# Kernel tuning notes

Hardware: AMD Instinct MI355X
Metric: run time of the kernel (lower is better)

Reference implementation:

```python
import jax, jax.numpy as jnp
import numpy as np

EPS = 1e-5


def _conv1x1_3d(x, w, b):
    # x: [B,C,T,H,W], w: [O,C], b: [O]  (Conv3d with kernel 1)
    return jnp.einsum('bcthw,oc->bothw', x, w) + b[None, :, None, None, None]


def _nonlocal_layer(x, Kw, Kb, Qw, Qb, Vw, Vb, Ow, Ob, gamma, beta, in_dim):
    K = _conv1x1_3d(x, Kw, Kb)
    Q = _conv1x1_3d(x, Qw, Qb)
    V = _conv1x1_3d(x, Vw, Vb)
    B, C, T, H, W = K.shape
    S = T * H * W
    Kf = K.reshape(B, C, S)
    Qf = Q.reshape(B, C, S)
    Vf = V.reshape(B, C, S)
    # KQ[b,s,t] = sum_c K[b,c,s] Q[b,c,t];  attn = softmax over t
    attn = jax.nn.softmax(jnp.einsum('bcs,bct->bst', Kf, Qf) / np.sqrt(in_dim).astype(np.float32), axis=2)
    # original broadcast pattern: (V.view(B,C,S,1) * attn[:,None]).sum(3)
    #   == V[b,c,s] * sum_t attn[b,s,t]  (rows of softmax sum to ~1)
    Vn = Vf * attn.sum(axis=2)[:, None, :]
    Vn = jax.nn.relu(Vn).reshape(B, C, T, H, W)
    O = jax.nn.relu(_conv1x1_3d(Vn, Ow, Ob))
    y = x + O
    # BatchNorm3d in training mode: per-channel batch statistics
    mu = y.mean(axis=(0, 2, 3, 4), keepdims=True)
    var = y.var(axis=(0, 2, 3, 4), keepdims=True)
    return gamma[None, :, None, None, None] * (y - mu) / jnp.sqrt(var + EPS) + beta[None, :, None, None, None]


def _conv_transpose_2x2_s2(x, w, b):
    # torch ConvTranspose2d(k=2, stride=2): weight [Cin, Cout, 2, 2]; output pixels don't overlap
    N, C, H, W = x.shape
    O = w.shape[1]
    y = jnp.einsum('nchw,codk->nohdwk', x, w).reshape(N, O, 2 * H, 2 * W)
    return y + b[None, :, None, None]


def _positional_encoding(S, D):
    position = jnp.arange(S, dtype=jnp.float32)[:, None]
    div_term = jnp.exp(jnp.arange(0, D, 2, dtype=jnp.float32) * (-np.log(10000.0) / D))
    pe = jnp.zeros((S, D), dtype=jnp.float32)
    pe = pe.at[:, 0::2].set(jnp.sin(position * div_term))
    pe = pe.at[:, 1::2].set(jnp.cos(position * div_term))
    return pe  # [S, D]


def setup_inputs() -> dict:
    key = jax.random.key(0)
    ks = jax.random.split(key, 24)
    B, Tc, Hc, Wc = 8, 6, 12, 12
    Tf, Hf, Wf = 4, 12, 12
    Din, Dff, Dout, L = 1024, 512, 128, 2
    s = 0.02
    inp = {
        'context': jax.random.normal(ks[0], (B, Tc, Din, Hc, Wc), jnp.float32),
        'frame': jax.random.normal(ks[1], (B, Tf, Din, Hf, Wf), jnp.float32),
        'nl_Kw': jax.random.normal(ks[2], (L, Dff, Din), jnp.float32) * s,
        'nl_Kb': jnp.zeros((L, Dff), jnp.float32),
        'nl_Qw': jax.random.normal(ks[3], (L, Dff, Din), jnp.float32) * s,
        'nl_Qb': jnp.zeros((L, Dff), jnp.float32),
        'nl_Vw': jax.random.normal(ks[4], (L, Dff, Din), jnp.float32) * s,
        'nl_Vb': jnp.zeros((L, Dff), jnp.float32),
        'nl_Ow': jax.random.normal(ks[5], (L, Din, Dff), jnp.float32) * s,
        'nl_Ob': jnp.zeros((L, Din), jnp.float32),
        'nl_gamma': jnp.ones((L, Din), jnp.float32),
        'nl_beta': jnp.zeros((L, Din), jnp.float32),
        'tp_w': jax.random.normal(ks[6], (Dout, Din, 3, 3, 3), jnp.float32) * s,
        'tp_b': jnp.zeros((Dout,), jnp.float32),
        'up1_w': jax.random.normal(ks[7], (Din, Dff, 2, 2), jnp.float32) * s,
        'up1_b': jnp.zeros((Dff,), jnp.float32),
        'up2_w': jax.random.normal(ks[8], (Dff, Dout, 2, 2), jnp.float32) * s,
        'up2_b': jnp.zeros((Dout,), jnp.float32),
    }
    return inp


def reference(context, frame, nl_Kw, nl_Kb, nl_Qw, nl_Qb, nl_Vw, nl_Vb, nl_Ow, nl_Ob,
              nl_gamma, nl_beta, tp_w, tp_b, up1_w, up1_b, up2_w, up2_b):
    in_dim = context.shape[2]
    out_dim = up2_w.shape[1]
    # ---- non-local layers over context ----
    x = jnp.swapaxes(context, 1, 2)  # [B, C, T, H, W]
    n_layers = nl_Kw.shape[0]
    for l in range(n_layers):
        x = _nonlocal_layer(x, nl_Kw[l], nl_Kb[l], nl_Qw[l], nl_Qb[l], nl_Vw[l], nl_Vb[l],
                            nl_Ow[l], nl_Ob[l], nl_gamma[l], nl_beta[l], in_dim)
    # ---- temporal pool (Conv3d k=3, VALID) + ReLU + global avg pool ----
    g = jax.lax.conv_general_dilated(x, tp_w, (1, 1, 1), 'VALID',
                                     dimension_numbers=('NCDHW', 'OIDHW', 'NCDHW'))
    g = jax.nn.relu(g + tp_b[None, :, None, None, None])
    goal_embed = g.mean(axis=(2, 3, 4))  # [B, out_dim]
    # ---- upsample frame ----
    B, Tf, C, H, W = frame.shape
    fr = frame.reshape(B * Tf, C, H, W)
    h = jax.nn.relu(_conv_transpose_2x2_s2(fr, up1_w, up1_b))
    h = _conv_transpose_2x2_s2(h, up2_w, up2_b)  # [B*Tf, out_dim, 4H, 4W]
    N = B * Tf
    S = H * W * 16
    state_embed = h.reshape(N, out_dim, S)
    # ---- positional encoding on V ----
    pe = _positional_encoding(S, out_dim)  # [S, D]
    V = jnp.transpose(state_embed, (0, 2, 1)) + pe[None, :, :]  # [N, S, D]
    # ---- goal/state attention (note: torch .repeat tiles t-major, kept faithful) ----
    goal_rep = jnp.tile(goal_embed, (Tf, 1))  # [Tf*B, D], index t*B+b
    SG = jnp.einsum('nds,nd->ns', state_embed, goal_rep) / np.sqrt(out_dim).astype(np.float32)
    attn = jax.nn.softmax(SG, axis=1)  # [N, S]
    state_goal_attn = jnp.einsum('ns,nsd->nd', attn, V).reshape(B, Tf, out_dim)
    return (goal_embed, state_goal_attn)
```

## Files before the change

### kernel.cpp

```cpp
#include <hip/hip_runtime.h>
#include <cstddef>
#include <cstdint>


static constexpr int B_ = 8, TC = 6, TF = 4, DIN = 1024, DFF = 512, DOUT = 128;
static constexpr int HWP = 144;
static constexpr int P_CTX = B_ * TC * HWP;
static constexpr int NF = B_ * TF;
static constexpr int P_FRM = NF * HWP;
static constexpr int P_H1 = NF * 24 * 24;
static constexpr int P_H2 = NF * 48 * 48;
static constexpr int S2 = 48 * 48;
static constexpr int NPOS = 3200;

static constexpr size_t OFF_XB   = 0;
static constexpr size_t OFF_YB   = 3538944;
static constexpr size_t OFF_VNB  = 7077888;
static constexpr size_t OFF_WB1  = 8847360;
static constexpr size_t OFF_WB2  = 9371648;
static constexpr size_t OFF_ST   = 9895936;
static constexpr size_t OFF_TWB  = 9900032;
static constexpr size_t OFF_W1B  = 11669504;
static constexpr size_t OFF_W2B  = 12718080;
static constexpr size_t OFF_GP   = 12849152;
static constexpr size_t OFF_R    = 18378752;
static constexpr size_t OFF_HP1B = 18788352;
static constexpr size_t OFF_F0B  = 23506944;
static constexpr size_t OFF_HP2B = 0;
static constexpr size_t OFF_SG   = 12849152;
static constexpr size_t OFF_PE   = 7077888;

typedef __attribute__((ext_vector_type(8))) short bf16x8;
typedef __attribute__((ext_vector_type(4))) float f32x4;
typedef __attribute__((ext_vector_type(4))) unsigned short us4;
typedef __attribute__((ext_vector_type(8))) unsigned short us8;

__device__ __forceinline__ unsigned short f2b(float f) {
    union { float f; uint32_t u; } x{f};
    uint32_t r = x.u + 0x7FFFu + ((x.u >> 16) & 1u);
    return (unsigned short)(r >> 16);
}
__device__ __forceinline__ float b2f(unsigned short u) {
    union { uint32_t u; float f; } x;
    x.u = (uint32_t)u << 16;
    return x.f;
}

#define GL16(g, s)                                                        \
    __builtin_amdgcn_global_load_lds(                                     \
        (const __attribute__((address_space(1))) void*)(g),               \
        (__attribute__((address_space(3))) void*)(s), 16, 0, 0)

static constexpr int PW0 = 4 * 524288;
static constexpr int PW1 = PW0 + 27 * 1024 * 128;
static constexpr int PW2 = PW1 + 4 * 512 * 1024;
static constexpr int PW3 = PW2 + 4 * 128 * 512;
static constexpr int NB_PREP = PW3 / 256;
static constexpr int NB_CTXT = 9 * 16 * (B_ * TC);
static constexpr int NB_FRMT = 9 * 16 * NF;

__device__ __forceinline__ void transpose_body(const float* __restrict__ in,
                                               unsigned short* __restrict__ outB,
                                               int C, int HW, int bx, int by, int bz,
                                               float (*T)[17]) {
    int tid = threadIdx.x;
    int tx = tid & 15, ty = tid >> 4;
    int f = bz, hw0 = bx * 16, c0 = by * 64;
#pragma unroll
    for (int i = 0; i < 4; ++i)
        T[ty + 16 * i][tx] = in[((size_t)f * C + c0 + ty + 16 * i) * HW + hw0 + tx];
    __syncthreads();
#pragma unroll
    for (int i = 0; i < 4; ++i)
        outB[((size_t)f * HW + hw0 + ty) * C + c0 + tx + 16 * i] = f2b(T[tx + 16 * i][ty]);
}

__global__ __launch_bounds__(256) void prep_all(
    const float* __restrict__ Vw, const float* __restrict__ Ow,
    const float* __restrict__ tp, const float* __restrict__ u1w,
    const float* __restrict__ u2w,
    const float* __restrict__ context, const float* __restrict__ frame,
    unsigned short* __restrict__ WB1, unsigned short* __restrict__ WB2,
    unsigned short* __restrict__ TWB, unsigned short* __restrict__ W1B,
    unsigned short* __restrict__ W2B,
    unsigned short* __restrict__ XB, unsigned short* __restrict__ F0B) {
    __shared__ float T[64][17];
    int b = blockIdx.x;
    if (b < NB_PREP) {
        int t = b * 256 + threadIdx.x;
        if (t < PW0) {
            int which = t >> 19;
            int r = t & 524287;
            int kr = r & 7;
            int layer = which >> 1;
            if ((which & 1) == 0) {
                int o = (r >> 3) & 511, kg = (r >> 3) >> 9;
                WB1[(size_t)layer * 524288 + r] =
                    f2b(Vw[(size_t)layer * 524288 + (size_t)o * 1024 + kg * 8 + kr]);
            } else {
                int o = (r >> 3) & 1023, kg = (r >> 3) >> 10;
                WB2[(size_t)layer * 524288 + r] =
                    f2b(Ow[(size_t)layer * 524288 + (size_t)o * 512 + kg * 8 + kr]);
            }
        } else if (t < PW1) {
            int r = t - PW0;
            int kr = r & 7, o = (r >> 3) & 127, kg = (r >> 10) & 127, tap = r >> 17;
            int c = kg * 8 + kr;
            TWB[r] = f2b(tp[((size_t)o * 1024 + c) * 27 + tap]);
        } else if (t < PW2) {
            int r = t - PW1;
            int kr = r & 7, o = (r >> 3) % 512;
            int rest = (r >> 3) / 512;
            int kg = rest & 127, d = rest >> 7;
            W1B[r] = f2b(u1w[((size_t)(kg * 8 + kr) * 512 + o) * 4 + d]);
        } else if (t < PW3) {
            int r = t - PW2;
            int kr = r & 7, o = (r >> 3) & 127;
            int rest = (r >> 3) >> 7;
            int kg = rest & 63, d = rest >> 6;
            W2B[r] = f2b(u2w[((size_t)(kg * 8 + kr) * 128 + o) * 4 + d]);
        }
    } else if (b < NB_PREP + NB_CTXT) {
        int bb = b - NB_PREP;
        transpose_body(context, XB, DIN, HWP, bb % 9, (bb / 9) % 16, bb / 144, T);
    } else {
        int bb = b - NB_PREP - NB_CTXT;
        transpose_body(frame, F0B, DIN, HWP, bb % 9, (bb / 9) % 16, bb / 144, T);
    }
}

template <int EPI, int REMAP, int GATHER, int MT>
__device__ __forceinline__ void gemm_body(
    const unsigned short* __restrict__ A, const unsigned short* __restrict__ Bp,
    const float* __restrict__ bias, const unsigned short* __restrict__ resid,
    void* __restrict__ Cv, int M, int N, int K,
    size_t bStrideZ, size_t cStrideZ,
    int inW, int inHW, int outW, int outSPP,
    int bx, int by, int bz,
    unsigned short* AlP, unsigned short* BlP, int* sPix) {
    constexpr int MI = MT / 32;
    constexpr int AL = MT / 64;
    constexpr int ASZ = MT * 32;
    int tid = threadIdx.x;
    int w = tid >> 6, l = tid & 63;
    int m0 = by * MT, n0 = bx * 128;
    int z = bz;
    const unsigned short* Bpz = Bp + (size_t)z * bStrideZ;

    if (GATHER) {
        if (tid < MT) {
            int pos = m0 + tid;
            int ww = pos % 10;
            int r = pos / 10;
            int h = r % 10;
            r /= 10;
            int t = r & 3, b = r >> 2;
            int dt = z / 9, rr = z - dt * 9;
            int doff = dt * 144 + (rr / 3) * 12 + (rr % 3);
            sPix[tid] = ((b * 6 + t) * 12 + h) * 12 + ww + doff;
        }
        __syncthreads();
    }

    int wr = w >> 1, wc = w & 1;
    int l15 = l & 15, lg = l >> 4;

    float bv[4];
#pragma unroll
    for (int ni = 0; ni < 4; ++ni)
        bv[ni] = (EPI & 1) ? bias[n0 + wc * 64 + ni * 16 + l15] : 0.f;
    asm volatile("s_waitcnt vmcnt(0)" ::: "memory");

    const unsigned short* ag[AL];
    int aoff[AL];
#pragma unroll
    for (int a = 0; a < AL; ++a) {
        int row = l + a * 64;
        int grow = GATHER ? sPix[row] : (m0 + row);
        ag[a] = A + (size_t)grow * K + w * 8;
        aoff[a] = (w * MT + row) * 8;
    }
    int bkg = tid >> 7, bn = tid & 127;
    const unsigned short* bg0 = Bpz + ((size_t)bkg * N + n0 + bn) * 8;
    const unsigned short* bg1 = Bpz + ((size_t)(bkg + 2) * N + n0 + bn) * 8;
    const int boff0 = tid * 8, boff1 = (tid + 256) * 8;
    size_t bstep = (size_t)32 * N;

    f32x4 acc[MI][4];
#pragma unroll
    for (int mi = 0; mi < MI; ++mi)
#pragma unroll
        for (int ni = 0; ni < 4; ++ni) acc[mi][ni] = (f32x4){0.f, 0.f, 0.f, 0.f};

    int nt = K >> 5;
#pragma unroll
    for (int a = 0; a < AL; ++a) { GL16(ag[a], &AlP[aoff[a]]); ag[a] += 32; }
    GL16(bg0, &BlP[boff0]);
    GL16(bg1, &BlP[boff1]);
    bg0 += bstep; bg1 += bstep;
#pragma unroll
    for (int a = 0; a < AL; ++a) { GL16(ag[a], &AlP[ASZ + aoff[a]]); ag[a] += 32; }
    GL16(bg0, &BlP[4096 + boff0]);
    GL16(bg1, &BlP[4096 + boff1]);
    bg0 += bstep; bg1 += bstep;

    int bc = 0, sb = 2;
    for (int t = 0; t < nt; ++t) {
        __builtin_amdgcn_s_barrier();
        if (t + 2 < nt) {
#pragma unroll
            for (int a = 0; a < AL; ++a) { GL16(ag[a], &AlP[sb * ASZ + aoff[a]]); ag[a] += 32; }
            GL16(bg0, &BlP[sb * 4096 + boff0]);
            GL16(bg1, &BlP[sb * 4096 + boff1]);
            bg0 += bstep; bg1 += bstep;
            if (MT == 128)
                asm volatile("s_waitcnt vmcnt(8)" ::: "memory");
            else
                asm volatile("s_waitcnt vmcnt(6)" ::: "memory");
        } else if (t + 2 == nt) {
            if (MT == 128)
                asm volatile("s_waitcnt vmcnt(4)" ::: "memory");
            else
                asm volatile("s_waitcnt vmcnt(3)" ::: "memory");
        } else {
            asm volatile("s_waitcnt vmcnt(0)" ::: "memory");
        }
        __builtin_amdgcn_sched_barrier(0);
        bf16x8 af[MI], bf[4];
#pragma unroll
        for (int mi = 0; mi < MI; ++mi)
            af[mi] = *(const bf16x8*)&AlP[bc * ASZ + (lg * MT + wr * (MT / 2) + mi * 16 + l15) * 8];
#pragma unroll
        for (int ni = 0; ni < 4; ++ni)
            bf[ni] = *(const bf16x8*)&BlP[bc * 4096 + (lg * 128 + wc * 64 + ni * 16 + l15) * 8];
        __builtin_amdgcn_s_setprio(1);
#pragma unroll
        for (int mi = 0; mi < MI; ++mi)
#pragma unroll
            for (int ni = 0; ni < 4; ++ni)
                acc[mi][ni] = __builtin_amdgcn_mfma_f32_16x16x32_bf16(
                    af[mi], bf[ni], acc[mi][ni], 0, 0, 0);
        __builtin_amdgcn_s_setprio(0);
        __builtin_amdgcn_sched_barrier(0);
        bc = (bc == 2) ? 0 : bc + 1;
        sb = (sb == 2) ? 0 : sb + 1;
    }

    float* Cf = (float*)Cv + (size_t)z * cStrideZ;
    unsigned short* Cb = (unsigned short*)Cv + (size_t)z * cStrideZ;
#pragma unroll
    for (int mi = 0; mi < MI; ++mi) {
#pragma unroll
        for (int r = 0; r < 4; ++r) {
            int m = m0 + wr * (MT / 2) + mi * 16 + lg * 4 + r;
            int orow = m;
            if (REMAP) {
                int ni_ = m / inHW;
                int rem = m - ni_ * inHW;
                int h = rem / inW, ww = rem - h * inW;
                orow = ni_ * outSPP + (2 * h + (z >> 1)) * outW + (2 * ww + (z & 1));
            }
#pragma unroll
            for (int ni = 0; ni < 4; ++ni) {
                int n = n0 + wc * 64 + ni * 16 + l15;
                float v = acc[mi][ni][r] + bv[ni];
                if (EPI & 2) v = fmaxf(v, 0.f);
                if (EPI & 4) v += b2f(resid[(size_t)m * N + n]);
                if (EPI & 8)
                    Cb[(size_t)orow * N + n] = f2b(v);
                else
                    Cf[(size_t)orow * N + n] = v;
            }
        }
    }
}

template <int EPI, int REMAP, int GATHER, int MT>
__global__ __launch_bounds__(256) void gemm_mfma(
    const unsigned short* __restrict__ A, const unsigned short* __restrict__ Bp,
    const float* __restrict__ bias, const unsigned short* __restrict__ resid,
    void* __restrict__ Cv, int M, int N, int K,
    size_t bStrideZ, size_t cStrideZ,
    int inW, int inHW, int outW, int outSPP) {
    __shared__ unsigned short Al[3 * MT * 32];
    __shared__ unsigned short Bl[3 * 128 * 32];
    __shared__ int sPix[MT];
    gemm_body<EPI, REMAP, GATHER, MT>(A, Bp, bias, resid, Cv, M, N, K,
                                      bStrideZ, cStrideZ, inW, inHW, outW, outSPP,
                                      blockIdx.x, blockIdx.y, blockIdx.z,
                                      Al, Bl, sPix);
}

__global__ __launch_bounds__(256) void conv3_up1(
    const unsigned short* __restrict__ XB, const unsigned short* __restrict__ TWB,
    unsigned short* __restrict__ GP,
    const unsigned short* __restrict__ F0B, const unsigned short* __restrict__ W1B,
    const float* __restrict__ u1b, unsigned short* __restrict__ HP1B) {
    __shared__ unsigned short Al[3 * 128 * 32];
    __shared__ unsigned short Bl[3 * 128 * 32];
    __shared__ int sPix[128];
    if (blockIdx.x < 680) {
        int xcd = blockIdx.x & 7, k = blockIdx.x >> 3;
        int wcnt = (xcd < 3) ? 85 : 84;
        if (k >= wcnt) return;
        int wk = (xcd < 3) ? xcd * 85 + k : 255 + (xcd - 3) * 84 + k;
        gemm_body<8, 0, 1, 128>(XB, TWB, nullptr, nullptr, GP, NPOS, DOUT, DIN,
                                (size_t)DIN / 8 * DOUT * 8, (size_t)NPOS * DOUT,
                                0, 0, 0, 0, 0, wk / 27, wk % 27, Al, Bl, sPix);
    } else {
        int b = blockIdx.x - 680;
        gemm_body<11, 1, 0, 128>(F0B, W1B, u1b, nullptr, HP1B, P_FRM, DFF, DIN,
                                 (size_t)DIN / 8 * DFF * 8, 0, 12, 144, 24, 576,
                                 b & 3, (b >> 2) % 36, b / 144, Al, Bl, sPix);
    }
}

__global__ __launch_bounds__(256) void up2_tail(
    const unsigned short* __restrict__ HP1B, const unsigned short* __restrict__ W2B,
    const float* __restrict__ u2b, unsigned short* __restrict__ HP2B,
    const unsigned short* __restrict__ Gp, const float* __restrict__ tpb,
    float* __restrict__ R, float* __restrict__ PE) {
    __shared__ unsigned short Al[3 * 128 * 32];
    __shared__ unsigned short Bl[3 * 128 * 32];
    __shared__ int sPix[128];
    int b = blockIdx.x;
    if (b < 576) {
        gemm_body<9, 1, 0, 128>(HP1B, W2B, u2b, nullptr, HP2B, P_H1, DOUT, DFF,
                                (size_t)DFF / 8 * DOUT * 8, 0, 24, 576, 48, 2304,
                                0, b % 144, b / 144, Al, Bl, sPix);
    } else if (b < 2176) {
        int idx = (b - 576) * 256 + threadIdx.x;
        float s = 0.f;
        for (int tap = 0; tap < 27; ++tap) s += b2f(Gp[(size_t)tap * (NPOS * 128) + idx]);
        R[idx] = fmaxf(s + tpb[idx & 127], 0.f);
    } else {
        int idx = (b - 2176) * 256 + threadIdx.x;
        int s = idx >> 7, d = idx & 127;
        float freq = expf(-(float)(d & ~1) * (9.210340371976184f / 128.f));
        float ang = (float)s * freq;
        PE[idx] = (d & 1) ? cosf(ang) : sinf(ang);
    }
}

__global__ __launch_bounds__(128) void goal_reduce(const float* __restrict__ R,
                                                   float* __restrict__ out) {
    int b = blockIdx.x, o = threadIdx.x;
    float s = 0.f;
    for (int i = 0; i < 400; ++i) s += R[(size_t)(b * 400 + i) * 128 + o];
    out[b * 128 + o] = s * (1.f / 400.f);
}


__global__ __launch_bounds__(256) void bn_stats_b(const unsigned short* __restrict__ YB,
                                                  float* __restrict__ st) {
    int tid = threadIdx.x;
    int p0 = blockIdx.x * 64;
    int c0 = tid * 4;
    float s[4] = {0, 0, 0, 0}, q[4] = {0, 0, 0, 0};
    for (int pp = 0; pp < 64; ++pp) {
        us4 y = *(const us4*)(YB + (size_t)(p0 + pp) * 1024 + c0);
#pragma unroll
        for (int j = 0; j < 4; ++j) {
            float v = b2f(y[j]);
            s[j] += v;
            q[j] += v * v;
        }
    }
#pragma unroll
    for (int j = 0; j < 4; ++j) {
        atomicAdd(&st[c0 + j], s[j]);
        atomicAdd(&st[1024 + c0 + j], q[j]);
    }
}

__global__ __launch_bounds__(256) void bn_final(float* __restrict__ st,
                                                const float* __restrict__ gamma,
                                                const float* __restrict__ beta) {
    int c = blockIdx.x * 256 + threadIdx.x;
    if (c >= 1024) return;
    const float invn = 1.f / 6912.f;
    float mean = st[c] * invn;
    float var = st[1024 + c] * invn - mean * mean;
    float sc = gamma[c] * rsqrtf(var + 1e-5f);
    st[2048 + c] = sc;
    st[3072 + c] = beta[c] - mean * sc;
}

__global__ __launch_bounds__(256) void bn_apply_b(const unsigned short* __restrict__ YB,
                                                  unsigned short* __restrict__ XB,
                                                  const float* __restrict__ st) {
    const float* scale = st + 2048;
    const float* shift = st + 3072;
    int idx = blockIdx.x * 256 + threadIdx.x;
    int c0 = (idx & 255) << 2;
    us4 y = ((const us4*)YB)[idx];
    us4 o;
#pragma unroll
    for (int j = 0; j < 4; ++j) o[j] = f2b(b2f(y[j]) * scale[c0 + j] + shift[c0 + j]);
    ((us4*)XB)[idx] = o;
}


__global__ __launch_bounds__(256) void attn_logits(const unsigned short* __restrict__ Hp2,
                                                   const float* __restrict__ out,
                                                   float* __restrict__ SG) {
    int n = blockIdx.y;
    int tid = threadIdx.x;
    int s = blockIdx.x * 16 + (tid >> 4);
    int l16 = tid & 15;
    us8 row = *((const us8*)(Hp2 + ((size_t)n * S2 + s) * 128) + l16);
    const float* g = out + (n & 7) * 128 + l16 * 8;
    float dot = 0.f;
#pragma unroll
    for (int i = 0; i < 8; ++i) dot += b2f(row[i]) * g[i];
    dot += __shfl_xor(dot, 1);
    dot += __shfl_xor(dot, 2);
    dot += __shfl_xor(dot, 4);
    dot += __shfl_xor(dot, 8);
    if (l16 == 0) SG[(size_t)n * S2 + s] = dot * 0.0883883476483184f;
}

__global__ __launch_bounds__(256) void attn_softmax(float* __restrict__ SG) {
    __shared__ float red[256];
    int n = blockIdx.x, tid = threadIdx.x;
    float* row = SG + (size_t)n * S2;
    float v[9];
    float lmax = -3.4e38f;
#pragma unroll
    for (int i = 0; i < 9; ++i) {
        v[i] = row[tid + 256 * i];
        lmax = fmaxf(lmax, v[i]);
    }
    red[tid] = lmax;
    __syncthreads();
    for (int off = 128; off > 0; off >>= 1) {
        if (tid < off) red[tid] = fmaxf(red[tid], red[tid + off]);
        __syncthreads();
    }
    float m = red[0];
    __syncthreads();
    float ls = 0.f;
#pragma unroll
    for (int i = 0; i < 9; ++i) {
        v[i] = expf(v[i] - m);
        ls += v[i];
    }
    red[tid] = ls;
    __syncthreads();
    for (int off = 128; off > 0; off >>= 1) {
        if (tid < off) red[tid] += red[tid + off];
        __syncthreads();
    }
    float inv = 1.f / red[0];
#pragma unroll
    for (int i = 0; i < 9; ++i) row[tid + 256 * i] = v[i] * inv;
}

__global__ __launch_bounds__(256) void attn_pv(const unsigned short* __restrict__ Hp2,
                                               const float* __restrict__ SG,
                                               const float* __restrict__ PE,
                                               float* __restrict__ out) {
    int n = blockIdx.y;
    int sb = blockIdx.x;
    int tid = threadIdx.x;
    int d = tid & 127, half = tid >> 7;
    int s0 = sb * 128 + half * 64;
    const float* att = SG + (size_t)n * S2;
    float acc = 0.f;
    for (int i = 0; i < 64; ++i) {
        int s = s0 + i;
        acc += att[s] * (b2f(Hp2[((size_t)n * S2 + s) * 128 + d]) + PE[(size_t)s * 128 + d]);
    }
    atomicAdd(&out[1024 + n * 128 + d], acc);
}


extern "C" void kernel_launch(void* const* d_in, const int* in_sizes, int n_in,
                              void* d_out, int out_size, void* d_ws, size_t ws_size,
                              hipStream_t stream) {
    const float* context = (const float*)d_in[0];
    const float* frame = (const float*)d_in[1];
    const float* Vw = (const float*)d_in[6];
    const float* Vb = (const float*)d_in[7];
    const float* Ow = (const float*)d_in[8];
    const float* Ob = (const float*)d_in[9];
    const float* gamma = (const float*)d_in[10];
    const float* beta = (const float*)d_in[11];
    const float* tpw = (const float*)d_in[12];
    const float* tpb = (const float*)d_in[13];
    const float* u1w = (const float*)d_in[14];
    const float* u1b = (const float*)d_in[15];
    const float* u2w = (const float*)d_in[16];
    const float* u2b = (const float*)d_in[17];
    float* ws = (float*)d_ws;
    float* out = (float*)d_out;

    unsigned short* XB = (unsigned short*)(ws + OFF_XB);
    unsigned short* YB = (unsigned short*)(ws + OFF_YB);
    unsigned short* VNB = (unsigned short*)(ws + OFF_VNB);
    unsigned short* WB1 = (unsigned short*)(ws + OFF_WB1);
    unsigned short* WB2 = (unsigned short*)(ws + OFF_WB2);
    float* ST = ws + OFF_ST;
    unsigned short* TWB = (unsigned short*)(ws + OFF_TWB);
    unsigned short* W1B = (unsigned short*)(ws + OFF_W1B);
    unsigned short* W2B = (unsigned short*)(ws + OFF_W2B);
    unsigned short* GP = (unsigned short*)(ws + OFF_GP);
    float* R = ws + OFF_R;
    unsigned short* F0B = (unsigned short*)(ws + OFF_F0B);
    unsigned short* HP1B = (unsigned short*)(ws + OFF_HP1B);
    unsigned short* HP2B = (unsigned short*)(ws + OFF_HP2B);
    float* SG = ws + OFF_SG;
    float* PE = ws + OFF_PE;

    prep_all<<<NB_PREP + NB_CTXT + NB_FRMT, 256, 0, stream>>>(
        Vw, Ow, tpw, u1w, u2w, context, frame, WB1, WB2, TWB, W1B, W2B, XB, F0B);

    for (int l = 0; l < 2; ++l) {
        gemm_mfma<11, 0, 0, 64><<<dim3(DFF / 128, P_CTX / 64, 1), 256, 0, stream>>>(
            XB, WB1 + (size_t)l * 524288, Vb + l * DFF, nullptr, VNB,
            P_CTX, DFF, DIN, 0, 0, 0, 0, 0, 0);
        gemm_mfma<15, 0, 0, 128><<<dim3(DIN / 128, P_CTX / 128, 1), 256, 0, stream>>>(
            VNB, WB2 + (size_t)l * 524288, Ob + l * DIN, XB, YB,
            P_CTX, DIN, DFF, 0, 0, 0, 0, 0, 0);
        hipMemsetAsync(ST, 0, 2048 * sizeof(float), stream);
        bn_stats_b<<<P_CTX / 64, 256, 0, stream>>>(YB, ST);
        bn_final<<<4, 256, 0, stream>>>(ST, gamma + l * DIN, beta + l * DIN);
        bn_apply_b<<<(P_CTX * DIN / 4) / 256, 256, 0, stream>>>(YB, XB, ST);
    }

    conv3_up1<<<680 + 576, 256, 0, stream>>>(XB, TWB, GP, F0B, W1B, u1b, HP1B);

    up2_tail<<<576 + 1600 + 1152, 256, 0, stream>>>(HP1B, W2B, u2b, HP2B,
                                                    GP, tpb, R, PE);
    goal_reduce<<<8, 128, 0, stream>>>(R, out);
    hipMemsetAsync(out + 1024, 0, (size_t)NF * 128 * sizeof(float), stream);

    attn_logits<<<dim3(S2 / 16, NF), 256, 0, stream>>>(HP2B, out, SG);
    attn_softmax<<<NF, 256, 0, stream>>>(SG);
    attn_pv<<<dim3(18, NF), 256, 0, stream>>>(HP2B, SG, PE, out);
}
```

Before: 286.4 us.

## Fuse BatchNorm statistics into GEMM epilogue and fold memsets into kernels

```diff
diff --git a/kernel.cpp b/kernel.cpp
--- a/kernel.cpp
+++ b/kernel.cpp
@@ -18,16 +18,16 @@
 static constexpr size_t OFF_VNB  = 7077888;
 static constexpr size_t OFF_WB1  = 8847360;
 static constexpr size_t OFF_WB2  = 9371648;
-static constexpr size_t OFF_ST   = 9895936;
 static constexpr size_t OFF_TWB  = 9900032;
 static constexpr size_t OFF_W1B  = 11669504;
 static constexpr size_t OFF_W2B  = 12718080;
+static constexpr size_t OFF_ST   = 12849152;
 static constexpr size_t OFF_GP   = 12849152;
 static constexpr size_t OFF_R    = 18378752;
 static constexpr size_t OFF_HP1B = 18788352;
 static constexpr size_t OFF_F0B  = 23506944;
 static constexpr size_t OFF_HP2B = 0;
-static constexpr size_t OFF_SG   = 12849152;
+static constexpr size_t OFF_SG   = 14692352;
 static constexpr size_t OFF_PE   = 7077888;
 
 typedef __attribute__((ext_vector_type(8))) short bf16x8;
@@ -58,6 +58,7 @@
 static constexpr int NB_PREP = PW3 / 256;
 static constexpr int NB_CTXT = 9 * 16 * (B_ * TC);
 static constexpr int NB_FRMT = 9 * 16 * NF;
+static constexpr int NB_STZ  = 32;
 
 __device__ __forceinline__ void transpose_body(const float* __restrict__ in,
                                                unsigned short* __restrict__ outB,
@@ -83,7 +84,8 @@
     unsigned short* __restrict__ WB1, unsigned short* __restrict__ WB2,
     unsigned short* __restrict__ TWB, unsigned short* __restrict__ W1B,
     unsigned short* __restrict__ W2B,
-    unsigned short* __restrict__ XB, unsigned short* __restrict__ F0B) {
+    unsigned short* __restrict__ XB, unsigned short* __restrict__ F0B,
+    float* __restrict__ ST) {
     __shared__ float T[64][17];
     int b = blockIdx.x;
     if (b < NB_PREP) {
@@ -123,9 +125,12 @@
     } else if (b < NB_PREP + NB_CTXT) {
         int bb = b - NB_PREP;
         transpose_body(context, XB, DIN, HWP, bb % 9, (bb / 9) % 16, bb / 144, T);
-    } else {
+    } else if (b < NB_PREP + NB_CTXT + NB_FRMT) {
         int bb = b - NB_PREP - NB_CTXT;
         transpose_body(frame, F0B, DIN, HWP, bb % 9, (bb / 9) % 16, bb / 144, T);
+    } else {
+        int idx = (b - NB_PREP - NB_CTXT - NB_FRMT) * 256 + threadIdx.x;
+        ST[idx] = 0.f;
     }
 }
 
@@ -133,7 +138,7 @@
 __device__ __forceinline__ void gemm_body(
     const unsigned short* __restrict__ A, const unsigned short* __restrict__ Bp,
     const float* __restrict__ bias, const unsigned short* __restrict__ resid,
-    void* __restrict__ Cv, int M, int N, int K,
+    void* __restrict__ Cv, float* __restrict__ stats, int M, int N, int K,
     size_t bStrideZ, size_t cStrideZ,
     int inW, int inHW, int outW, int outSPP,
     int bx, int by, int bz,
@@ -248,6 +253,7 @@
 
     float* Cf = (float*)Cv + (size_t)z * cStrideZ;
     unsigned short* Cb = (unsigned short*)Cv + (size_t)z * cStrideZ;
+    float sacc[4] = {0, 0, 0, 0}, qacc[4] = {0, 0, 0, 0};
 #pragma unroll
     for (int mi = 0; mi < MI; ++mi) {
 #pragma unroll
@@ -266,6 +272,7 @@
                 float v = acc[mi][ni][r] + bv[ni];
                 if (EPI & 2) v = fmaxf(v, 0.f);
                 if (EPI & 4) v += b2f(resid[(size_t)m * N + n]);
+                if (EPI & 16) { sacc[ni] += v; qacc[ni] += v * v; }
                 if (EPI & 8)
                     Cb[(size_t)orow * N + n] = f2b(v);
                 else
@@ -273,19 +280,36 @@
             }
         }
     }
+    if (EPI & 16) {
+        __syncthreads();
+        float* sred = (float*)AlP;
+        sred[tid] = 0.f;
+        __syncthreads();
+#pragma unroll
+        for (int ni = 0; ni < 4; ++ni) {
+            int c = wc * 64 + ni * 16 + l15;
+            atomicAdd(&sred[c], sacc[ni]);
+            atomicAdd(&sred[128 + c], qacc[ni]);
+        }
+        __syncthreads();
+        if (tid < 128)
+            atomicAdd(&stats[n0 + tid], sred[tid]);
+        else
+            atomicAdd(&stats[1024 + n0 + (tid & 127)], sred[tid]);
+    }
 }
 
 template <int EPI, int REMAP, int GATHER, int MT>
 __global__ __launch_bounds__(256) void gemm_mfma(
     const unsigned short* __restrict__ A, const unsigned short* __restrict__ Bp,
     const float* __restrict__ bias, const unsigned short* __restrict__ resid,
-    void* __restrict__ Cv, int M, int N, int K,
+    void* __restrict__ Cv, float* __restrict__ stats, int M, int N, int K,
     size_t bStrideZ, size_t cStrideZ,
     int inW, int inHW, int outW, int outSPP) {
     __shared__ unsigned short Al[3 * MT * 32];
     __shared__ unsigned short Bl[3 * 128 * 32];
     __shared__ int sPix[MT];
-    gemm_body<EPI, REMAP, GATHER, MT>(A, Bp, bias, resid, Cv, M, N, K,
+    gemm_body<EPI, REMAP, GATHER, MT>(A, Bp, bias, resid, Cv, stats, M, N, K,
                                       bStrideZ, cStrideZ, inW, inHW, outW, outSPP,
                                       blockIdx.x, blockIdx.y, blockIdx.z,
                                       Al, Bl, sPix);
@@ -304,12 +328,14 @@
         int wcnt = (xcd < 3) ? 85 : 84;
         if (k >= wcnt) return;
         int wk = (xcd < 3) ? xcd * 85 + k : 255 + (xcd - 3) * 84 + k;
-        gemm_body<8, 0, 1, 128>(XB, TWB, nullptr, nullptr, GP, NPOS, DOUT, DIN,
+        gemm_body<8, 0, 1, 128>(XB, TWB, nullptr, nullptr, GP, nullptr,
+                                NPOS, DOUT, DIN,
                                 (size_t)DIN / 8 * DOUT * 8, (size_t)NPOS * DOUT,
                                 0, 0, 0, 0, 0, wk / 27, wk % 27, Al, Bl, sPix);
     } else {
         int b = blockIdx.x - 680;
-        gemm_body<11, 1, 0, 128>(F0B, W1B, u1b, nullptr, HP1B, P_FRM, DFF, DIN,
+        gemm_body<11, 1, 0, 128>(F0B, W1B, u1b, nullptr, HP1B, nullptr,
+                                 P_FRM, DFF, DIN,
                                  (size_t)DIN / 8 * DFF * 8, 0, 12, 144, 24, 576,
                                  b & 3, (b >> 2) % 36, b / 144, Al, Bl, sPix);
     }
@@ -319,13 +345,14 @@
     const unsigned short* __restrict__ HP1B, const unsigned short* __restrict__ W2B,
     const float* __restrict__ u2b, unsigned short* __restrict__ HP2B,
     const unsigned short* __restrict__ Gp, const float* __restrict__ tpb,
-    float* __restrict__ R, float* __restrict__ PE) {
+    float* __restrict__ R, float* __restrict__ PE, float* __restrict__ out) {
     __shared__ unsigned short Al[3 * 128 * 32];
     __shared__ unsigned short Bl[3 * 128 * 32];
     __shared__ int sPix[128];
     int b = blockIdx.x;
     if (b < 576) {
-        gemm_body<9, 1, 0, 128>(HP1B, W2B, u2b, nullptr, HP2B, P_H1, DOUT, DFF,
+        gemm_body<9, 1, 0, 128>(HP1B, W2B, u2b, nullptr, HP2B, nullptr,
+                                P_H1, DOUT, DFF,
                                 (size_t)DFF / 8 * DOUT * 8, 0, 24, 576, 48, 2304,
                                 0, b % 144, b / 144, Al, Bl, sPix);
     } else if (b < 2176) {
@@ -333,12 +360,15 @@
         float s = 0.f;
         for (int tap = 0; tap < 27; ++tap) s += b2f(Gp[(size_t)tap * (NPOS * 128) + idx]);
         R[idx] = fmaxf(s + tpb[idx & 127], 0.f);
-    } else {
+    } else if (b < 3328) {
         int idx = (b - 2176) * 256 + threadIdx.x;
         int s = idx >> 7, d = idx & 127;
         float freq = expf(-(float)(d & ~1) * (9.210340371976184f / 128.f));
         float ang = (float)s * freq;
         PE[idx] = (d & 1) ? cosf(ang) : sinf(ang);
+    } else {
+        int idx = (b - 3328) * 256 + threadIdx.x;
+        out[1024 + idx] = 0.f;
     }
 }
 
@@ -350,28 +380,6 @@
     out[b * 128 + o] = s * (1.f / 400.f);
 }
 
-
-__global__ __launch_bounds__(256) void bn_stats_b(const unsigned short* __restrict__ YB,
-                                                  float* __restrict__ st) {
-    int tid = threadIdx.x;
-    int p0 = blockIdx.x * 64;
-    int c0 = tid * 4;
-    float s[4] = {0, 0, 0, 0}, q[4] = {0, 0, 0, 0};
-    for (int pp = 0; pp < 64; ++pp) {
-        us4 y = *(const us4*)(YB + (size_t)(p0 + pp) * 1024 + c0);
-#pragma unroll
-        for (int j = 0; j < 4; ++j) {
-            float v = b2f(y[j]);
-            s[j] += v;
-            q[j] += v * v;
-        }
-    }
-#pragma unroll
-    for (int j = 0; j < 4; ++j) {
-        atomicAdd(&st[c0 + j], s[j]);
-        atomicAdd(&st[1024 + c0 + j], q[j]);
-    }
-}
 
 __global__ __launch_bounds__(256) void bn_final(float* __restrict__ st,
                                                 const float* __restrict__ gamma,
@@ -512,28 +520,27 @@
     float* SG = ws + OFF_SG;
     float* PE = ws + OFF_PE;
 
-    prep_all<<<NB_PREP + NB_CTXT + NB_FRMT, 256, 0, stream>>>(
-        Vw, Ow, tpw, u1w, u2w, context, frame, WB1, WB2, TWB, W1B, W2B, XB, F0B);
+    prep_all<<<NB_PREP + NB_CTXT + NB_FRMT + NB_STZ, 256, 0, stream>>>(
+        Vw, Ow, tpw, u1w, u2w, context, frame, WB1, WB2, TWB, W1B, W2B,
+        XB, F0B, ST);
 
     for (int l = 0; l < 2; ++l) {
+        float* STl = ST + (size_t)l * 4096;
         gemm_mfma<11, 0, 0, 64><<<dim3(DFF / 128, P_CTX / 64, 1), 256, 0, stream>>>(
-            XB, WB1 + (size_t)l * 524288, Vb + l * DFF, nullptr, VNB,
+            XB, WB1 + (size_t)l * 524288, Vb + l * DFF, nullptr, VNB, nullptr,
             P_CTX, DFF, DIN, 0, 0, 0, 0, 0, 0);
-        gemm_mfma<15, 0, 0, 128><<<dim3(DIN / 128, P_CTX / 128, 1), 256, 0, stream>>>(
-            VNB, WB2 + (size_t)l * 524288, Ob + l * DIN, XB, YB,
+        gemm_mfma<31, 0, 0, 128><<<dim3(DIN / 128, P_CTX / 128, 1), 256, 0, stream>>>(
+            VNB, WB2 + (size_t)l * 524288, Ob + l * DIN, XB, YB, STl,
             P_CTX, DIN, DFF, 0, 0, 0, 0, 0, 0);
-        hipMemsetAsync(ST, 0, 2048 * sizeof(float), stream);
-        bn_stats_b<<<P_CTX / 64, 256, 0, stream>>>(YB, ST);
-        bn_final<<<4, 256, 0, stream>>>(ST, gamma + l * DIN, beta + l * DIN);
-        bn_apply_b<<<(P_CTX * DIN / 4) / 256, 256, 0, stream>>>(YB, XB, ST);
+        bn_final<<<4, 256, 0, stream>>>(STl, gamma + l * DIN, beta + l * DIN);
+        bn_apply_b<<<(P_CTX * DIN / 4) / 256, 256, 0, stream>>>(YB, XB, STl);
     }
 
     conv3_up1<<<680 + 576, 256, 0, stream>>>(XB, TWB, GP, F0B, W1B, u1b, HP1B);
 
-    up2_tail<<<576 + 1600 + 1152, 256, 0, stream>>>(HP1B, W2B, u2b, HP2B,
-                                                    GP, tpb, R, PE);
+    up2_tail<<<576 + 1600 + 1152 + 16, 256, 0, stream>>>(HP1B, W2B, u2b, HP2B,
+                                                         GP, tpb, R, PE, out);
     goal_reduce<<<8, 128, 0, stream>>>(R, out);
-    hipMemsetAsync(out + 1024, 0, (size_t)NF * 128 * sizeof(float), stream);
 
     attn_logits<<<dim3(S2 / 16, NF), 256, 0, stream>>>(HP2B, out, SG);
     attn_softmax<<<NF, 256, 0, stream>>>(SG);
```

New measurement: 262.6 us. -8.3%, faster.
